# Performance work log

Measured on AMD Instinct MI355X. Metric: run time of the kernel, lower is better.

## Reference

```python
import jax, jax.numpy as jnp
import numpy as np

B, S, D = 8, 512, 384
VOCAB = 50257


def setup_inputs() -> dict:
    key = jax.random.key(0)
    ks = jax.random.split(key, 8)
    tokens = jax.random.randint(ks[0], (B, S), 0, VOCAB)
    dep_types = jax.random.randint(ks[1], (B, S), 0, 64)
    dep_heads = jax.random.randint(ks[2], (B, S), 0, S)
    tok_table = jax.random.normal(ks[3], (VOCAB, D), dtype=jnp.float32) * 0.02
    # composition bilinear: out[o] = x1 @ Wc[o] @ x2 + bc[o]
    Wc = jax.random.normal(ks[4], (D, D, D), dtype=jnp.float32) * (1.0 / np.sqrt(D))
    bc = jax.random.normal(ks[5], (D,), dtype=jnp.float32) * 0.01
    # reduction Linear(seq_len, 1): weight (1, S), bias (1,)
    Wr = jax.random.normal(ks[6], (1, S), dtype=jnp.float32) * (1.0 / np.sqrt(S))
    br = jax.random.normal(ks[7], (1,), dtype=jnp.float32) * 0.01
    return {"tokens": tokens, "dep_types": dep_types, "dep_heads": dep_heads,
            "tok_table": tok_table, "Wc": Wc, "bc": bc, "Wr": Wr, "br": br}


def _composition_block(tok, heads, Wc, bc, Wr, br):
    # Original math (with the dep_transform-overwrite bug preserved):
    #   dep = tanh(tok)                                   [B,S,D]
    #   expanded[b,s1,s2,:] = tok[b,s2,:]
    #   masked_dep[b,s1,s2,:] = dep[b,s2,:] * (heads[b,s2]==s1)
    #   comp[b,s1,s2,o] = tanh(bilinear(tok[b,s2], masked_dep[b,s1,s2]))[o]
    #   y[b,s1,o] = sum_s2 Wr[0,s2]*comp[b,s1,s2,o] + br[0]
    # Since masked_dep is zero unless heads[b,s2]==s1, bilinear reduces to
    # bias-only (t_off) off-tree and full value (t_on) on-tree -> O(S) scatter.
    dep = jnp.tanh(tok)
    u = jnp.einsum('bsd,ode,bse->bso', tok, Wc, dep)      # [B,S,D] full bilinear value
    t_on = jnp.tanh(u + bc)                               # [B,S,D]
    t_off = jnp.tanh(bc)                                  # [D]
    w = Wr[0]                                             # [S]
    base = t_off * jnp.sum(w) + br[0]                     # [D]
    contrib = (t_on - t_off) * w[None, :, None]           # [B,S,D]
    scat = jax.vmap(lambda h, c: jnp.zeros((S, D), dtype=tok.dtype).at[h].add(c))(heads, contrib)
    return scat + base[None, None, :]                     # [B,S,D]


def reference(tokens, dep_types, dep_heads, tok_table, Wc, bc, Wr, br):
    depth = 1
    tok = tok_table[tokens]                               # [B,S,D]
    # dep_types embedding is computed in the original but its result is
    # discarded inside the block (bug); it does not affect the output.
    for _ in range(depth):
        tok = _composition_block(tok, dep_heads, Wc, bc, Wr, br)
    out_mask = (dep_heads == 0)[:, :, None]               # [B,S,1]
    return tok * out_mask.astype(tok.dtype)
```

## Files before the change

### kernel.cpp

```cpp
#include <hip/hip_runtime.h>

#define BB 8
#define SS 512
#define DD 384
#define K2 (DD * DD)
#define LCH 16
#define OT 2
#define KCH 4
#define GROUPS (K2 / 4)
#define GPC (GROUPS / KCH)
#define NT 512
#define ITERS (GPC / NT)
#define MAXL_CAP 1024

#define WS_LIST_OFF 16
#define WS_U_OFF 16400

__global__ void flag_kernel(const int* __restrict__ heads, int* __restrict__ countp,
                            int* __restrict__ list, int maxl) {
    int b = blockIdx.x;
    int s2 = threadIdx.x;
    int h = heads[b * SS + s2];
    if (heads[b * SS + h] == 0) {
        int idx = atomicAdd(countp, 1);
        if (idx < maxl) list[idx] = b * SS + s2;
    }
}

__global__ __launch_bounds__(NT, 6) void bilinear_kernel(
    const float* __restrict__ Wc, const float* __restrict__ tok_table,
    const int* __restrict__ tokens, const int* __restrict__ list,
    const int* __restrict__ countp, float* __restrict__ u, int maxl) {
    __shared__ alignas(16) float tokS[LCH][DD];
    __shared__ alignas(16) float depS[LCH][DD];

    const int tid = threadIdx.x;
    const int o0 = blockIdx.x * OT;
    const int g0 = blockIdx.y * GPC;

    int total = *countp;
    if (total > maxl) total = maxl;

    for (int cb = 0; cb < total; cb += LCH) {
        for (int idx = tid; idx < LCH * DD; idx += NT) {
            int l = idx / DD;
            int i = idx - l * DD;
            float t = 0.f;
            if (cb + l < total) {
                int pos = list[cb + l];
                t = tok_table[(size_t)tokens[pos] * DD + i];
            }
            tokS[l][i] = t;
            depS[l][i] = tanhf(t);
        }
        __syncthreads();

        float acc[LCH][OT];
#pragma unroll
        for (int l = 0; l < LCH; ++l)
#pragma unroll
            for (int j = 0; j < OT; ++j) acc[l][j] = 0.f;

        const float* wbase = Wc + (size_t)o0 * K2;
        float4 wv0, wv1;
        {
            const float* wp = wbase + 4 * (size_t)(g0 + tid);
            wv0 = *(const float4*)wp;
            wv1 = *(const float4*)(wp + K2);
        }

#pragma unroll 1
        for (int it = 0; it < ITERS; ++it) {
            int gc = g0 + it * NT + tid;

            float4 nv0 = make_float4(0.f, 0.f, 0.f, 0.f), nv1 = nv0;
            if (it + 1 < ITERS) {
                const float* wp = wbase + 4 * (size_t)(gc + NT);
                nv0 = *(const float4*)wp;
                nv1 = *(const float4*)(wp + K2);
            }

            int d = gc / 96;
            int e4 = gc - d * 96;

#pragma unroll
            for (int l = 0; l < LCH; ++l) {
                float td = tokS[l][d];
                float4 dv = *(const float4*)(&depS[l][e4 * 4]);
                float px = td * dv.x, py = td * dv.y, pz = td * dv.z, pw = td * dv.w;
                acc[l][0] += px * wv0.x + py * wv0.y + pz * wv0.z + pw * wv0.w;
                acc[l][1] += px * wv1.x + py * wv1.y + pz * wv1.z + pw * wv1.w;
            }
            wv0 = nv0;
            wv1 = nv1;
        }

        int lane = tid & 63;
#pragma unroll
        for (int l = 0; l < LCH; ++l) {
            if (cb + l < total) {
#pragma unroll
                for (int j = 0; j < OT; ++j) {
                    float v = acc[l][j];
                    for (int off = 32; off > 0; off >>= 1) v += __shfl_down(v, off, 64);
                    if (lane == 0)
                        atomicAdd(&u[(size_t)(cb + l) * DD + o0 + j], v);
                }
            }
        }
        __syncthreads();
    }
}

__global__ __launch_bounds__(128) void finalize_kernel(
    const int* __restrict__ heads, const float* __restrict__ Wr,
    const float* __restrict__ bc, const float* __restrict__ br,
    const int* __restrict__ list, const int* __restrict__ countp,
    const float* __restrict__ u, float* __restrict__ out, int maxl) {
    int row = blockIdx.x;
    int tid = threadIdx.x;
    if (heads[row] != 0) {
        if (tid < DD / 4) {
            float4 z = make_float4(0.f, 0.f, 0.f, 0.f);
            ((float4*)(out + (size_t)row * DD))[tid] = z;
        }
        return;
    }
    int b = row >> 9;
    int s1 = row & 511;

    float sumw = 0.f;
    for (int s = 0; s < SS; ++s) sumw += Wr[s];
    float brv = br[0];

    int total = *countp;
    if (total > maxl) total = maxl;

    for (int o = tid; o < DD; o += 128) {
        float bco = bc[o];
        float t_off = tanhf(bco);
        float val = t_off * sumw + brv;
        for (int l = 0; l < total; ++l) {
            int pos = list[l];
            if ((pos >> 9) == b && heads[pos] == s1) {
                val += (tanhf(u[(size_t)l * DD + o] + bco) - t_off) * Wr[pos & 511];
            }
        }
        out[(size_t)row * DD + o] = val;
    }
}

extern "C" void kernel_launch(void* const* d_in, const int* in_sizes, int n_in,
                              void* d_out, int out_size, void* d_ws, size_t ws_size,
                              hipStream_t stream) {
    const int* tokens = (const int*)d_in[0];
    const int* heads = (const int*)d_in[2];
    const float* tok_table = (const float*)d_in[3];
    const float* Wc = (const float*)d_in[4];
    const float* bc = (const float*)d_in[5];
    const float* Wr = (const float*)d_in[6];
    const float* br = (const float*)d_in[7];
    float* out = (float*)d_out;

    char* ws = (char*)d_ws;
    int* countp = (int*)ws;
    int* list = (int*)(ws + WS_LIST_OFF);
    float* u = (float*)(ws + WS_U_OFF);

    long maxl_l = ((long)ws_size - WS_U_OFF) / (DD * 4);
    int maxl = maxl_l < 0 ? 0 : (maxl_l > MAXL_CAP ? MAXL_CAP : (int)maxl_l);

    hipMemsetAsync(d_ws, 0, (size_t)WS_U_OFF + (size_t)maxl * DD * 4, stream);

    flag_kernel<<<BB, SS, 0, stream>>>(heads, countp, list, maxl);
    bilinear_kernel<<<dim3(DD / OT, KCH), NT, 0, stream>>>(
        Wc, tok_table, tokens, list, countp, u, maxl);
    finalize_kernel<<<BB * SS, 128, 0, stream>>>(
        heads, Wr, bc, br, list, countp, u, out, maxl);
}
```

Baseline: 392.8 us.

## Replace atomics with per-chunk partials, drop memset, restructure bilinear K loop

The flag kernel becomes a single-wave ballot compaction, which writes the list in deterministic order, and the large workspace memset is removed. The bilinear kernel splits K into 8 chunks of 384 threads so each thread keeps its dep float4 values in registers across the loop. It reduces partials through shared memory and writes one value per chunk instead of doing global atomics, and finalize sums the 8 partials. This trades memset and atomic traffic for more finalize reads, and the single-wave flag kernel runs serially over all 4096 positions.

```diff
diff --git a/kernel.cpp b/kernel.cpp
--- a/kernel.cpp
+++ b/kernel.cpp
@@ -6,37 +6,48 @@
 #define K2 (DD * DD)
 #define LCH 16
 #define OT 2
-#define KCH 4
-#define GROUPS (K2 / 4)
-#define GPC (GROUPS / KCH)
-#define NT 512
-#define ITERS (GPC / NT)
-#define MAXL_CAP 1024
+#define KCH 8
+#define CHUNK_K (K2 / KCH)
+#define NT 384
+#define ITERS (CHUNK_K / (4 * DD))
+#define MAXL_CAP 4096
 
 #define WS_LIST_OFF 16
 #define WS_U_OFF 16400
 
 __global__ void flag_kernel(const int* __restrict__ heads, int* __restrict__ countp,
                             int* __restrict__ list, int maxl) {
-    int b = blockIdx.x;
-    int s2 = threadIdx.x;
-    int h = heads[b * SS + s2];
-    if (heads[b * SS + h] == 0) {
-        int idx = atomicAdd(countp, 1);
-        if (idx < maxl) list[idx] = b * SS + s2;
+    int lane = threadIdx.x;
+    int cnt = 0;
+    for (int base = 0; base < BB * SS; base += 64) {
+        int pos = base + lane;
+        int b = pos >> 9;
+        int h = heads[pos];
+        bool c = (heads[(b << 9) + h] == 0);
+        unsigned long long m = __ballot(c);
+        if (c) {
+            int off = cnt + (int)__popcll(m & ((1ull << lane) - 1ull));
+            if (off < maxl) list[off] = pos;
+        }
+        cnt += (int)__popcll(m);
     }
+    if (lane == 0) *countp = cnt > maxl ? maxl : cnt;
 }
 
-__global__ __launch_bounds__(NT, 6) void bilinear_kernel(
+__global__ __launch_bounds__(NT) void bilinear_kernel(
     const float* __restrict__ Wc, const float* __restrict__ tok_table,
     const int* __restrict__ tokens, const int* __restrict__ list,
-    const int* __restrict__ countp, float* __restrict__ u, int maxl) {
+    const int* __restrict__ countp, float* __restrict__ u_part, int maxl) {
     __shared__ alignas(16) float tokS[LCH][DD];
     __shared__ alignas(16) float depS[LCH][DD];
+    __shared__ float redS[NT / 64][LCH * OT];
 
     const int tid = threadIdx.x;
     const int o0 = blockIdx.x * OT;
-    const int g0 = blockIdx.y * GPC;
+    const int cb0 = blockIdx.y * CHUNK_K;
+    const int dbase = blockIdx.y * (CHUNK_K / DD);
+    const int dsub = tid / 96;
+    const int e4 = tid - dsub * 96;
 
     int total = *countp;
     if (total > maxl) total = maxl;
@@ -55,58 +66,58 @@
         }
         __syncthreads();
 
+        float4 dv[LCH];
+#pragma unroll
+        for (int l = 0; l < LCH; ++l) dv[l] = *(const float4*)(&depS[l][e4 * 4]);
+
         float acc[LCH][OT];
 #pragma unroll
         for (int l = 0; l < LCH; ++l)
 #pragma unroll
             for (int j = 0; j < OT; ++j) acc[l][j] = 0.f;
 
-        const float* wbase = Wc + (size_t)o0 * K2;
-        float4 wv0, wv1;
-        {
-            const float* wp = wbase + 4 * (size_t)(g0 + tid);
-            wv0 = *(const float4*)wp;
-            wv1 = *(const float4*)(wp + K2);
-        }
+        const float* wbase = Wc + (size_t)o0 * K2 + cb0 + tid * 4;
+        float4 wv0 = *(const float4*)wbase;
+        float4 wv1 = *(const float4*)(wbase + K2);
 
 #pragma unroll 1
         for (int it = 0; it < ITERS; ++it) {
-            int gc = g0 + it * NT + tid;
-
             float4 nv0 = make_float4(0.f, 0.f, 0.f, 0.f), nv1 = nv0;
             if (it + 1 < ITERS) {
-                const float* wp = wbase + 4 * (size_t)(gc + NT);
+                const float* wp = wbase + (it + 1) * (4 * DD);
                 nv0 = *(const float4*)wp;
                 nv1 = *(const float4*)(wp + K2);
             }
-
-            int d = gc / 96;
-            int e4 = gc - d * 96;
-
+            int d = dbase + it * 4 + dsub;
 #pragma unroll
             for (int l = 0; l < LCH; ++l) {
-                float td = tokS[l][d];
-                float4 dv = *(const float4*)(&depS[l][e4 * 4]);
-                float px = td * dv.x, py = td * dv.y, pz = td * dv.z, pw = td * dv.w;
-                acc[l][0] += px * wv0.x + py * wv0.y + pz * wv0.z + pw * wv0.w;
-                acc[l][1] += px * wv1.x + py * wv1.y + pz * wv1.z + pw * wv1.w;
+                float tv = tokS[l][d];
+                float s0 = dv[l].x * wv0.x + dv[l].y * wv0.y + dv[l].z * wv0.z + dv[l].w * wv0.w;
+                float s1 = dv[l].x * wv1.x + dv[l].y * wv1.y + dv[l].z * wv1.z + dv[l].w * wv1.w;
+                acc[l][0] += tv * s0;
+                acc[l][1] += tv * s1;
             }
             wv0 = nv0;
             wv1 = nv1;
         }
 
-        int lane = tid & 63;
+        int wid = tid >> 6, lane = tid & 63;
 #pragma unroll
-        for (int l = 0; l < LCH; ++l) {
-            if (cb + l < total) {
+        for (int l = 0; l < LCH; ++l)
 #pragma unroll
-                for (int j = 0; j < OT; ++j) {
-                    float v = acc[l][j];
-                    for (int off = 32; off > 0; off >>= 1) v += __shfl_down(v, off, 64);
-                    if (lane == 0)
-                        atomicAdd(&u[(size_t)(cb + l) * DD + o0 + j], v);
-                }
+            for (int j = 0; j < OT; ++j) {
+                float v = acc[l][j];
+                for (int off = 32; off > 0; off >>= 1) v += __shfl_down(v, off, 64);
+                if (lane == 0) redS[wid][l * OT + j] = v;
             }
+        __syncthreads();
+        if (tid < LCH * OT) {
+            float v = 0.f;
+#pragma unroll
+            for (int w = 0; w < NT / 64; ++w) v += redS[w][tid];
+            int l = tid / OT, j = tid - l * OT;
+            if (cb + l < total)
+                u_part[((size_t)blockIdx.y * maxl + (cb + l)) * DD + o0 + j] = v;
         }
         __syncthreads();
     }
@@ -116,7 +127,7 @@
     const int* __restrict__ heads, const float* __restrict__ Wr,
     const float* __restrict__ bc, const float* __restrict__ br,
     const int* __restrict__ list, const int* __restrict__ countp,
-    const float* __restrict__ u, float* __restrict__ out, int maxl) {
+    const float* __restrict__ u_part, float* __restrict__ out, int maxl) {
     int row = blockIdx.x;
     int tid = threadIdx.x;
     if (heads[row] != 0) {
@@ -143,7 +154,11 @@
         for (int l = 0; l < total; ++l) {
             int pos = list[l];
             if ((pos >> 9) == b && heads[pos] == s1) {
-                val += (tanhf(u[(size_t)l * DD + o] + bco) - t_off) * Wr[pos & 511];
+                float uv = 0.f;
+#pragma unroll
+                for (int kc = 0; kc < KCH; ++kc)
+                    uv += u_part[((size_t)kc * maxl + l) * DD + o];
+                val += (tanhf(uv + bco) - t_off) * Wr[pos & 511];
             }
         }
         out[(size_t)row * DD + o] = val;
@@ -165,16 +180,14 @@
     char* ws = (char*)d_ws;
     int* countp = (int*)ws;
     int* list = (int*)(ws + WS_LIST_OFF);
-    float* u = (float*)(ws + WS_U_OFF);
+    float* u_part = (float*)(ws + WS_U_OFF);
 
-    long maxl_l = ((long)ws_size - WS_U_OFF) / (DD * 4);
+    long maxl_l = ((long)ws_size - WS_U_OFF) / ((long)KCH * DD * 4);
     int maxl = maxl_l < 0 ? 0 : (maxl_l > MAXL_CAP ? MAXL_CAP : (int)maxl_l);
 
-    hipMemsetAsync(d_ws, 0, (size_t)WS_U_OFF + (size_t)maxl * DD * 4, stream);
-
-    flag_kernel<<<BB, SS, 0, stream>>>(heads, countp, list, maxl);
+    flag_kernel<<<1, 64, 0, stream>>>(heads, countp, list, maxl);
     bilinear_kernel<<<dim3(DD / OT, KCH), NT, 0, stream>>>(
-        Wc, tok_table, tokens, list, countp, u, maxl);
+        Wc, tok_table, tokens, list, countp, u_part, maxl);
     finalize_kernel<<<BB * SS, 128, 0, stream>>>(
-        heads, Wr, bc, br, list, countp, u, out, maxl);
+        heads, Wr, bc, br, list, countp, u_part, out, maxl);
 }
```

New measurement: 457.9 us. +16.6%, slower.
